# Performance work log

Hardware: AMD Instinct MI355X
Metric: run time of the kernel (lower is better)

## Reference

```python
import jax, jax.numpy as jnp
import numpy as np

B, CIN, COUT = 4, 64, 64
D, H, W = 8, 48, 48
KD = KH = KW = 3
K = KD * KH * KW  # 27 sampling taps
STRIDE, PAD, DIL = 1, 1, 1
KOFF, POFF = 3, 1
OFFSET_SCALE = 1.0


def setup_inputs() -> dict:
    key = jax.random.key(0)
    ks = jax.random.split(key, 7)
    x = jax.random.normal(ks[0], (B, CIN, D, H, W), jnp.float32)
    w_off = jax.random.normal(ks[1], (K * 3, CIN, KOFF, KOFF, KOFF), jnp.float32) * 0.01
    b_off = jax.random.normal(ks[2], (K * 3,), jnp.float32) * 0.01
    w_mask = jax.random.normal(ks[3], (K, CIN, KOFF, KOFF, KOFF), jnp.float32) * 0.05
    b_mask = jax.random.normal(ks[4], (K,), jnp.float32) * 0.05
    weight = jax.random.normal(ks[5], (COUT, CIN, KD, KH, KW), jnp.float32) * 0.02
    bias = jax.random.normal(ks[6], (COUT,), jnp.float32) * 0.02
    return dict(x=x, w_off=w_off, b_off=b_off, w_mask=w_mask, b_mask=b_mask,
                weight=weight, bias=bias)


def _conv3d(x, w, b, pad):
    out = jax.lax.conv_general_dilated(
        x, w, window_strides=(1, 1, 1), padding=[(pad, pad)] * 3,
        dimension_numbers=('NCDHW', 'OIDHW', 'NCDHW'))
    return out + b[None, :, None, None, None]


def _trilinear(x_flat, pz, py, px):
    # x_flat: [B, C, N]; pz/py/px: [B, N] fractional positions. Zero padding outside.
    z0, y0, x0 = jnp.floor(pz), jnp.floor(py), jnp.floor(px)
    acc = jnp.zeros_like(x_flat)
    for dz in (0.0, 1.0):
        for dy in (0.0, 1.0):
            for dx in (0.0, 1.0):
                zi, yi, xi = z0 + dz, y0 + dy, x0 + dx
                wgt = ((1.0 - jnp.abs(pz - zi)) * (1.0 - jnp.abs(py - yi))
                       * (1.0 - jnp.abs(px - xi)))
                valid = ((zi >= 0) & (zi < D) & (yi >= 0) & (yi < H)
                         & (xi >= 0) & (xi < W)).astype(x_flat.dtype)
                idx = ((jnp.clip(zi, 0, D - 1) * H + jnp.clip(yi, 0, H - 1)) * W
                       + jnp.clip(xi, 0, W - 1)).astype(jnp.int32)
                g = jnp.take_along_axis(x_flat, idx[:, None, :], axis=2)  # [B,C,N]
                acc = acc + g * (wgt * valid)[:, None, :]
    return acc


def reference(x, w_off, b_off, w_mask, b_mask, weight, bias):
    N = D * H * W
    # learned per-tap 3D offsets: [K, B, 3, N] ordered (dz, dy, dx)
    off = _conv3d(x, w_off, b_off, POFF).reshape(B, K, 3, N)
    off = jnp.transpose(off, (1, 0, 2, 3))
    # DCNv3-style attention mask: softmax over the K taps
    mask = jax.nn.softmax(_conv3d(x, w_mask, b_mask, POFF).reshape(B, K, N), axis=1)
    mask = jnp.transpose(mask, (1, 0, 2))  # [K, B, N]
    zo, yo, xo = jnp.meshgrid(jnp.arange(D, dtype=jnp.float32),
                              jnp.arange(H, dtype=jnp.float32),
                              jnp.arange(W, dtype=jnp.float32), indexing='ij')
    zo, yo, xo = zo.reshape(-1), yo.reshape(-1), xo.reshape(-1)  # [N]
    k_idx = jnp.arange(K)
    kz = (k_idx // (KH * KW)).astype(jnp.float32)
    ky = ((k_idx // KW) % KH).astype(jnp.float32)
    kx = (k_idx % KW).astype(jnp.float32)
    wk = jnp.transpose(weight.reshape(COUT, CIN, K), (2, 0, 1))  # [K, Cout, Cin]
    x_flat = x.reshape(B, CIN, N)

    def step(acc, inp):
        off_k, m_k, kzf, kyf, kxf, w_k = inp
        pz = zo[None] * STRIDE - PAD + kzf * DIL + OFFSET_SCALE * off_k[:, 0]
        py = yo[None] * STRIDE - PAD + kyf * DIL + OFFSET_SCALE * off_k[:, 1]
        px = xo[None] * STRIDE - PAD + kxf * DIL + OFFSET_SCALE * off_k[:, 2]
        s = _trilinear(x_flat, pz, py, px) * m_k[:, None, :]  # [B,Cin,N]
        return acc + jnp.einsum('oi,bin->bon', w_k, s), None

    acc0 = jnp.zeros((B, COUT, N), x.dtype)
    acc, _ = jax.lax.scan(step, acc0, (off, mask, kz, ky, kx, wk))
    return (acc + bias[None, :, None]).reshape(B, COUT, D, H, W)
```

## Files before the change

kernel.cpp:

```cpp
#include <hip/hip_runtime.h>
#include <hip/hip_bf16.h>
#include <math.h>

#define B_    4
#define CIN_  64
#define COUT_ 64
#define DD    8
#define HH    48
#define WW    48
#define HW2   (HH * WW)
#define NN    (DD * HH * WW)
#define BN    (B_ * NN)
#define KK    27
#define RS    116

typedef float f32x2 __attribute__((ext_vector_type(2)));
typedef float f32x4 __attribute__((ext_vector_type(4)));
typedef unsigned int u32x4 __attribute__((ext_vector_type(4)));
typedef __bf16 bf16x8 __attribute__((ext_vector_type(8)));
typedef __hip_bfloat16 bf16_t;

__device__ __forceinline__ float bflo(unsigned int u) {
  return __uint_as_float(u << 16);
}
__device__ __forceinline__ float bfhi(unsigned int u) {
  return __uint_as_float(u & 0xffff0000u);
}

__global__ __launch_bounds__(256) void init_kernel(
    const float* __restrict__ w_off, const float* __restrict__ w_mask,
    const float* __restrict__ weight, bf16_t* __restrict__ wB,
    bf16_t* __restrict__ wBd, bf16_t* __restrict__ zp)
{
  const int o = blockIdx.x * 256 + threadIdx.x;
  {
    const int ci = o & 63;
    const int ch = (o >> 6) % 112;
    const int k  = o / (112 * 64);
    float v = 0.f;
    if (ch < 81)       v = w_off[((size_t)ch * CIN_ + ci) * KK + k];
    else if (ch < 108) v = w_mask[((size_t)(ch - 81) * CIN_ + ci) * KK + k];
    wB[o] = __float2bfloat16(v);
  }
  if (o < KK * CIN_ * COUT_) {
    const int ci = o & 63;
    const int co = (o >> 6) & 63;
    const int k  = o >> 12;
    wBd[o] = __float2bfloat16(weight[((size_t)co * CIN_ + ci) * KK + k]);
  }
  if (o < 128) zp[o] = __float2bfloat16(0.f);
}

__global__ __launch_bounds__(256) void transpose_x_kernel(
    const float* __restrict__ x, bf16_t* __restrict__ xTbf)
{
  const int tid = threadIdx.x;
  const int n0  = blockIdx.x * 64;
  const int b   = blockIdx.y;
  __shared__ float tile[64][65];

  for (int i = tid; i < 4096; i += 256) {
    const int c  = i >> 6;
    const int nl = i & 63;
    tile[c][nl] = x[((size_t)(b * CIN_ + c)) * NN + n0 + nl];
  }
  __syncthreads();
  for (int i = tid; i < 4096; i += 256) {
    const int nl = i >> 6;
    const int c  = i & 63;
    xTbf[((size_t)(b * NN + n0 + nl)) * CIN_ + c] = __float2bfloat16(tile[c][nl]);
  }
}

__global__ __launch_bounds__(128) void fused_kernel(
    const bf16_t* __restrict__ xTbf, const bf16_t* __restrict__ wB,
    const float* __restrict__ b_off, const float* __restrict__ b_mask,
    const bf16_t* __restrict__ zp, const bf16_t* __restrict__ wBd,
    const float* __restrict__ bias, float* __restrict__ out)
{
  const int bid  = (blockIdx.x % 8) * 144 + blockIdx.x / 8;
  const int tid  = threadIdx.x;
  const int wid  = tid >> 6;
  const int lane = tid & 63;
  const int lg   = lane >> 4;
  const int lr   = lane & 15;

  const int tile = bid * 2 + wid;
  const int b    = tile / 576;
  const int rem  = tile % 576;
  const int z    = rem / 72;
  const int r2   = rem % 72;
  const int y0   = (r2 / 3) * 2;
  const int x0   = (r2 % 3) * 16;
  const int n0   = (z * HH + y0) * WW + x0;

  __shared__ float OM[2][32][RS];
  __shared__ __align__(16) unsigned short S[2][32][64];

  const bf16_t* xb = xTbf + (size_t)b * NN * CIN_;

  f32x4 acc[2][7];
#pragma unroll
  for (int mf = 0; mf < 2; ++mf)
#pragma unroll
    for (int nf = 0; nf < 7; ++nf) acc[mf][nf] = (f32x4){0.f, 0.f, 0.f, 0.f};

#pragma unroll 3
  for (int k = 0; k < KK; ++k) {
    const int kz = k / 9;
    const int kr = k - kz * 9;
    const int ky = kr / 3;
    const int kx = kr - ky * 3;

    bf16x8 afr[2][2];
    const int zz = z + kz - 1;
    const int xx = x0 + lr + kx - 1;
    const bool vzx = ((unsigned)zz < (unsigned)DD) & ((unsigned)xx < (unsigned)WW);
#pragma unroll
    for (int mf = 0; mf < 2; ++mf) {
      const int yy = y0 + mf + ky - 1;
      const bool v = vzx & ((unsigned)yy < (unsigned)HH);
      const bf16_t* ab = v ? (xb + (size_t)((zz * HH + yy) * WW + xx) * CIN_) : zp;
      afr[mf][0] = *(const bf16x8*)(ab + 8 * lg);
      afr[mf][1] = *(const bf16x8*)(ab + 32 + 8 * lg);
    }

    const bf16_t* wk = wB + (size_t)k * (112 * 64) + lr * 64 + 8 * lg;
#pragma unroll
    for (int nf = 0; nf < 7; ++nf) {
      const bf16x8 b0 = *(const bf16x8*)(wk + nf * 1024);
      const bf16x8 b1 = *(const bf16x8*)(wk + nf * 1024 + 32);
      acc[0][nf] = __builtin_amdgcn_mfma_f32_16x16x32_bf16(afr[0][0], b0, acc[0][nf], 0, 0, 0);
      acc[1][nf] = __builtin_amdgcn_mfma_f32_16x16x32_bf16(afr[1][0], b0, acc[1][nf], 0, 0, 0);
      acc[0][nf] = __builtin_amdgcn_mfma_f32_16x16x32_bf16(afr[0][1], b1, acc[0][nf], 0, 0, 0);
      acc[1][nf] = __builtin_amdgcn_mfma_f32_16x16x32_bf16(afr[1][1], b1, acc[1][nf], 0, 0, 0);
    }
  }

#pragma unroll
  for (int nf = 0; nf < 7; ++nf) {
    const int ch = 16 * nf + lr;
    if (ch < 108) {
      const float bv  = (ch < 81) ? b_off[ch] : b_mask[ch - 81];
      const int   slot = (ch < 81) ? (4 * (ch / 3) + (ch % 3)) : (4 * (ch - 81) + 3);
#pragma unroll
      for (int mf = 0; mf < 2; ++mf)
#pragma unroll
        for (int r = 0; r < 4; ++r)
          OM[wid][mf * 16 + 4 * lg + r][slot] = acc[mf][nf][r] + bv;
    }
  }
  __syncthreads();

  if (lane < 32) {
    const int pos = lane;
    float v[KK];
    float mx = -1e30f;
#pragma unroll
    for (int k = 0; k < KK; ++k) { v[k] = OM[wid][pos][4 * k + 3]; mx = fmaxf(mx, v[k]); }
    float s = 0.f;
#pragma unroll
    for (int k = 0; k < KK; ++k) { v[k] = expf(v[k] - mx); s += v[k]; }
    const float inv = 1.f / s;
#pragma unroll
    for (int k = 0; k < KK; ++k) OM[wid][pos][4 * k + 3] = v[k] * inv;
  }
  __syncthreads();

  const int p8 = lane >> 3;
  const int q  = lane & 7;

  const unsigned short* xq = (const unsigned short*)xb + (q << 3);
  unsigned short* Sw  = &S[wid][0][0];
  unsigned int*   SwU = (unsigned int*)Sw;

  float pxb[4], pyb[4];
#pragma unroll
  for (int oct = 0; oct < 4; ++oct) {
    const int j  = oct * 8 + p8;
    pyb[oct] = (float)(y0 + (j >> 4) - 1);
    pxb[oct] = (float)(x0 + (j & 15) - 1);
  }
  const float pzb = (float)(z - 1);

  f32x4 dacc[2][4];
#pragma unroll
  for (int mf = 0; mf < 2; ++mf)
#pragma unroll
    for (int nf = 0; nf < 4; ++nf) dacc[mf][nf] = (f32x4){0.f, 0.f, 0.f, 0.f};

#pragma unroll 2
  for (int k = 0; k < KK; ++k) {
    const int kz = k / 9;
    const int kr = k - kz * 9;
    const int ky = kr / 3;
    const int kx = kr - ky * 3;
    const float kzf = (float)kz, kyf = (float)ky, kxf = (float)kx;

#pragma unroll
    for (int oct = 0; oct < 4; ++oct) {
      const int j = oct * 8 + p8;
      const f32x4 om = *(const f32x4*)(&OM[wid][j][4 * k]);

      const float pz = pzb + kzf + om.x;
      const float py = pyb[oct] + kyf + om.y;
      const float px = pxb[oct] + kxf + om.z;
      const float m  = om.w;

      const float zf = floorf(pz); const float fz = pz - zf; const int z0 = (int)zf;
      const float yf = floorf(py); const float fy = py - yf; const int y0i = (int)yf;
      const float xf = floorf(px); const float fx = px - xf; const int xi0 = (int)xf;

      const float wz0 = ((unsigned)z0        < DD) ? (1.f - fz) : 0.f;
      const float wz1 = ((unsigned)(z0 + 1)  < DD) ? fz         : 0.f;
      const float wy0 = ((unsigned)y0i       < HH) ? (1.f - fy) : 0.f;
      const float wy1 = ((unsigned)(y0i + 1) < HH) ? fy         : 0.f;
      const float wx0 = ((unsigned)xi0       < WW) ? (1.f - fx) : 0.f;
      const float wx1 = ((unsigned)(xi0 + 1) < WW) ? fx         : 0.f;

      const int z0c = min(max(z0, 0),      DD - 1);
      const int z1c = min(max(z0 + 1, 0),  DD - 1);
      const int y0c = min(max(y0i, 0),     HH - 1);
      const int y1c = min(max(y0i + 1, 0), HH - 1);
      const int x0c = min(max(xi0, 0),     WW - 1);
      const int x1c = min(max(xi0 + 1, 0), WW - 1);

      const int r00 = (z0c * HH + y0c) * WW;
      const int r01 = (z0c * HH + y1c) * WW;
      const int r10 = (z1c * HH + y0c) * WW;
      const int r11 = (z1c * HH + y1c) * WW;

      const int rows[8] = {r00 + x0c, r00 + x1c, r01 + x0c, r01 + x1c,
                           r10 + x0c, r10 + x1c, r11 + x0c, r11 + x1c};
      const float w00 = wz0 * wy0, w01 = wz0 * wy1;
      const float w10 = wz1 * wy0, w11 = wz1 * wy1;
      const float wgt[8] = {w00 * wx0, w00 * wx1, w01 * wx0, w01 * wx1,
                            w10 * wx0, w10 * wx1, w11 * wx0, w11 * wx1};

      u32x4 cv[8];
#pragma unroll
      for (int c = 0; c < 8; ++c)
        cv[c] = *(const u32x4*)(xq + ((size_t)rows[c] << 6));

      f32x2 a01 = {0.f, 0.f}, a23 = {0.f, 0.f}, a45 = {0.f, 0.f}, a67 = {0.f, 0.f};
#pragma unroll
      for (int c = 0; c < 8; ++c) {
        const float w_ = wgt[c];
        a01 += (f32x2){bflo(cv[c].x), bfhi(cv[c].x)} * w_;
        a23 += (f32x2){bflo(cv[c].y), bfhi(cv[c].y)} * w_;
        a45 += (f32x2){bflo(cv[c].z), bfhi(cv[c].z)} * w_;
        a67 += (f32x2){bflo(cv[c].w), bfhi(cv[c].w)} * w_;
      }

      a01 *= m; a23 *= m; a45 *= m; a67 *= m;
      unsigned int d0, d1, d2, d3;
      asm("v_cvt_pk_bf16_f32 %0, %1, %2" : "=v"(d0) : "v"(a01.x), "v"(a01.y));
      asm("v_cvt_pk_bf16_f32 %0, %1, %2" : "=v"(d1) : "v"(a23.x), "v"(a23.y));
      asm("v_cvt_pk_bf16_f32 %0, %1, %2" : "=v"(d2) : "v"(a45.x), "v"(a45.y));
      asm("v_cvt_pk_bf16_f32 %0, %1, %2" : "=v"(d3) : "v"(a67.x), "v"(a67.y));
      const int slot = q ^ (j & 7);
      *(u32x4*)(SwU + j * 32 + slot * 4) = (u32x4){d0, d1, d2, d3};
    }

    bf16x8 afr2[2][2];
#pragma unroll
    for (int mf = 0; mf < 2; ++mf)
#pragma unroll
      for (int t2 = 0; t2 < 2; ++t2) {
        const int row  = 16 * mf + lr;
        const int slot = (t2 * 4 + lg) ^ (row & 7);
        afr2[mf][t2] = *(const bf16x8*)(Sw + row * 64 + slot * 8);
      }
    const bf16_t* wk = wBd + (size_t)k * 4096 + lr * 64 + 8 * lg;
#pragma unroll
    for (int nf = 0; nf < 4; ++nf) {
      const bf16x8 wv0 = *(const bf16x8*)(wk + nf * 1024);
      const bf16x8 wv1 = *(const bf16x8*)(wk + nf * 1024 + 32);
      dacc[0][nf] = __builtin_amdgcn_mfma_f32_16x16x32_bf16(afr2[0][0], wv0, dacc[0][nf], 0, 0, 0);
      dacc[1][nf] = __builtin_amdgcn_mfma_f32_16x16x32_bf16(afr2[1][0], wv0, dacc[1][nf], 0, 0, 0);
      dacc[0][nf] = __builtin_amdgcn_mfma_f32_16x16x32_bf16(afr2[0][1], wv1, dacc[0][nf], 0, 0, 0);
      dacc[1][nf] = __builtin_amdgcn_mfma_f32_16x16x32_bf16(afr2[1][1], wv1, dacc[1][nf], 0, 0, 0);
    }
  }

#pragma unroll
  for (int nf = 0; nf < 4; ++nf) {
    const float bv = bias[16 * nf + lr];
    float* op = out + ((size_t)(b * COUT_ + 16 * nf + lr)) * NN + n0 + 4 * lg;
#pragma unroll
    for (int mf = 0; mf < 2; ++mf)
      *(f32x4*)(op + mf * WW) = dacc[mf][nf] + bv;
  }
}

extern "C" void kernel_launch(void* const* d_in, const int* in_sizes, int n_in,
                              void* d_out, int out_size, void* d_ws, size_t ws_size,
                              hipStream_t stream)
{
  const float* x      = (const float*)d_in[0];
  const float* w_off  = (const float*)d_in[1];
  const float* b_off  = (const float*)d_in[2];
  const float* w_mask = (const float*)d_in[3];
  const float* b_mask = (const float*)d_in[4];
  const float* weight = (const float*)d_in[5];
  const float* bias   = (const float*)d_in[6];
  float* out = (float*)d_out;

  char* ws = (char*)d_ws;
  bf16_t* xTbf = (bf16_t*)ws;
  bf16_t* wB   = (bf16_t*)(ws + 9437184);
  bf16_t* wBd  = (bf16_t*)(ws + 9824256);
  bf16_t* zp   = (bf16_t*)(ws + 10045440);

  init_kernel<<<(KK * 112 * 64) / 256, 256, 0, stream>>>(w_off, w_mask, weight,
                                                         wB, wBd, zp);
  dim3 gtx(NN / 64, B_);
  transpose_x_kernel<<<gtx, 256, 0, stream>>>(x, xTbf);

  fused_kernel<<<1152, 128, 0, stream>>>(xTbf, wB, b_off, b_mask, zp, wBd,
                                         bias, out);
}
```

Measured before the change: 319.3 us.

## Halve per-wave tile to 16 positions and store offsets/mask as fp16 in LDS

Each wave now handles one 16-wide row segment instead of a 2x16 block, so the grid doubles to 2304 blocks and per-thread accumulators and fragments shrink by half. The offset/mask staging buffer moves from fp32 to fp16, which cuts shared-memory use. Together these lower register and LDS pressure to allow more resident waves and more parallelism. The cost is that each weight load from global memory now feeds half as many MFMAs, and the fp16 rounding of offsets and mask weights adds precision error.

```diff
diff --git a/kernel.cpp b/kernel.cpp
--- a/kernel.cpp
+++ b/kernel.cpp
@@ -12,10 +12,10 @@
 #define NN    (DD * HH * WW)
 #define BN    (B_ * NN)
 #define KK    27
-#define RS    116
 
 typedef float f32x2 __attribute__((ext_vector_type(2)));
 typedef float f32x4 __attribute__((ext_vector_type(4)));
+typedef unsigned int u32x2 __attribute__((ext_vector_type(2)));
 typedef unsigned int u32x4 __attribute__((ext_vector_type(4)));
 typedef __bf16 bf16x8 __attribute__((ext_vector_type(8)));
 typedef __hip_bfloat16 bf16_t;
@@ -25,6 +25,13 @@
 }
 __device__ __forceinline__ float bfhi(unsigned int u) {
   return __uint_as_float(u & 0xffff0000u);
+}
+__device__ __forceinline__ unsigned short f32_to_h(float x) {
+  _Float16 h = (_Float16)x;
+  return __builtin_bit_cast(unsigned short, h);
+}
+__device__ __forceinline__ float h_to_f32(unsigned short u) {
+  return (float)__builtin_bit_cast(_Float16, u);
 }
 
 __global__ __launch_bounds__(256) void init_kernel(
@@ -78,7 +85,7 @@
     const bf16_t* __restrict__ zp, const bf16_t* __restrict__ wBd,
     const float* __restrict__ bias, float* __restrict__ out)
 {
-  const int bid  = (blockIdx.x % 8) * 144 + blockIdx.x / 8;
+  const int bid  = (blockIdx.x % 8) * 288 + blockIdx.x / 8;
   const int tid  = threadIdx.x;
   const int wid  = tid >> 6;
   const int lane = tid & 63;
@@ -86,24 +93,22 @@
   const int lr   = lane & 15;
 
   const int tile = bid * 2 + wid;
-  const int b    = tile / 576;
-  const int rem  = tile % 576;
-  const int z    = rem / 72;
-  const int r2   = rem % 72;
-  const int y0   = (r2 / 3) * 2;
+  const int b    = tile / 1152;
+  const int rem  = tile % 1152;
+  const int z    = rem / 144;
+  const int r2   = rem % 144;
+  const int y    = r2 / 3;
   const int x0   = (r2 % 3) * 16;
-  const int n0   = (z * HH + y0) * WW + x0;
-
-  __shared__ float OM[2][32][RS];
-  __shared__ __align__(16) unsigned short S[2][32][64];
+  const int n0   = (z * HH + y) * WW + x0;
+
+  __shared__ __align__(16) unsigned short OMh[2][16][112];
+  __shared__ __align__(16) unsigned short S[2][16][64];
 
   const bf16_t* xb = xTbf + (size_t)b * NN * CIN_;
 
-  f32x4 acc[2][7];
-#pragma unroll
-  for (int mf = 0; mf < 2; ++mf)
-#pragma unroll
-    for (int nf = 0; nf < 7; ++nf) acc[mf][nf] = (f32x4){0.f, 0.f, 0.f, 0.f};
+  f32x4 acc[7];
+#pragma unroll
+  for (int nf = 0; nf < 7; ++nf) acc[nf] = (f32x4){0.f, 0.f, 0.f, 0.f};
 
 #pragma unroll 3
   for (int k = 0; k < KK; ++k) {
@@ -112,28 +117,23 @@
     const int ky = kr / 3;
     const int kx = kr - ky * 3;
 
-    bf16x8 afr[2][2];
     const int zz = z + kz - 1;
+    const int yy = y + ky - 1;
     const int xx = x0 + lr + kx - 1;
-    const bool vzx = ((unsigned)zz < (unsigned)DD) & ((unsigned)xx < (unsigned)WW);
-#pragma unroll
-    for (int mf = 0; mf < 2; ++mf) {
-      const int yy = y0 + mf + ky - 1;
-      const bool v = vzx & ((unsigned)yy < (unsigned)HH);
-      const bf16_t* ab = v ? (xb + (size_t)((zz * HH + yy) * WW + xx) * CIN_) : zp;
-      afr[mf][0] = *(const bf16x8*)(ab + 8 * lg);
-      afr[mf][1] = *(const bf16x8*)(ab + 32 + 8 * lg);
-    }
+    const bool v = ((unsigned)zz < (unsigned)DD) &
+                   ((unsigned)yy < (unsigned)HH) &
+                   ((unsigned)xx < (unsigned)WW);
+    const bf16_t* ab = v ? (xb + (size_t)((zz * HH + yy) * WW + xx) * CIN_) : zp;
+    const bf16x8 a0 = *(const bf16x8*)(ab + 8 * lg);
+    const bf16x8 a1 = *(const bf16x8*)(ab + 32 + 8 * lg);
 
     const bf16_t* wk = wB + (size_t)k * (112 * 64) + lr * 64 + 8 * lg;
 #pragma unroll
     for (int nf = 0; nf < 7; ++nf) {
       const bf16x8 b0 = *(const bf16x8*)(wk + nf * 1024);
       const bf16x8 b1 = *(const bf16x8*)(wk + nf * 1024 + 32);
-      acc[0][nf] = __builtin_amdgcn_mfma_f32_16x16x32_bf16(afr[0][0], b0, acc[0][nf], 0, 0, 0);
-      acc[1][nf] = __builtin_amdgcn_mfma_f32_16x16x32_bf16(afr[1][0], b0, acc[1][nf], 0, 0, 0);
-      acc[0][nf] = __builtin_amdgcn_mfma_f32_16x16x32_bf16(afr[0][1], b1, acc[0][nf], 0, 0, 0);
-      acc[1][nf] = __builtin_amdgcn_mfma_f32_16x16x32_bf16(afr[1][1], b1, acc[1][nf], 0, 0, 0);
+      acc[nf] = __builtin_amdgcn_mfma_f32_16x16x32_bf16(a0, b0, acc[nf], 0, 0, 0);
+      acc[nf] = __builtin_amdgcn_mfma_f32_16x16x32_bf16(a1, b1, acc[nf], 0, 0, 0);
     }
   }
 
@@ -141,29 +141,31 @@
   for (int nf = 0; nf < 7; ++nf) {
     const int ch = 16 * nf + lr;
     if (ch < 108) {
-      const float bv  = (ch < 81) ? b_off[ch] : b_mask[ch - 81];
+      const float bv   = (ch < 81) ? b_off[ch] : b_mask[ch - 81];
       const int   slot = (ch < 81) ? (4 * (ch / 3) + (ch % 3)) : (4 * (ch - 81) + 3);
 #pragma unroll
-      for (int mf = 0; mf < 2; ++mf)
-#pragma unroll
-        for (int r = 0; r < 4; ++r)
-          OM[wid][mf * 16 + 4 * lg + r][slot] = acc[mf][nf][r] + bv;
+      for (int r = 0; r < 4; ++r)
+        OMh[wid][4 * lg + r][slot] = f32_to_h(acc[nf][r] + bv);
     }
   }
   __syncthreads();
 
-  if (lane < 32) {
+  if (lane < 16) {
     const int pos = lane;
     float v[KK];
     float mx = -1e30f;
 #pragma unroll
-    for (int k = 0; k < KK; ++k) { v[k] = OM[wid][pos][4 * k + 3]; mx = fmaxf(mx, v[k]); }
+    for (int k = 0; k < KK; ++k) {
+      v[k] = h_to_f32(OMh[wid][pos][4 * k + 3]);
+      mx = fmaxf(mx, v[k]);
+    }
     float s = 0.f;
 #pragma unroll
     for (int k = 0; k < KK; ++k) { v[k] = expf(v[k] - mx); s += v[k]; }
     const float inv = 1.f / s;
 #pragma unroll
-    for (int k = 0; k < KK; ++k) OM[wid][pos][4 * k + 3] = v[k] * inv;
+    for (int k = 0; k < KK; ++k)
+      OMh[wid][pos][4 * k + 3] = f32_to_h(v[k] * inv);
   }
   __syncthreads();
 
@@ -174,20 +176,12 @@
   unsigned short* Sw  = &S[wid][0][0];
   unsigned int*   SwU = (unsigned int*)Sw;
 
-  float pxb[4], pyb[4];
-#pragma unroll
-  for (int oct = 0; oct < 4; ++oct) {
-    const int j  = oct * 8 + p8;
-    pyb[oct] = (float)(y0 + (j >> 4) - 1);
-    pxb[oct] = (float)(x0 + (j & 15) - 1);
-  }
   const float pzb = (float)(z - 1);
-
-  f32x4 dacc[2][4];
-#pragma unroll
-  for (int mf = 0; mf < 2; ++mf)
-#pragma unroll
-    for (int nf = 0; nf < 4; ++nf) dacc[mf][nf] = (f32x4){0.f, 0.f, 0.f, 0.f};
+  const float pyb = (float)(y - 1);
+
+  f32x4 dacc[4];
+#pragma unroll
+  for (int nf = 0; nf < 4; ++nf) dacc[nf] = (f32x4){0.f, 0.f, 0.f, 0.f};
 
 #pragma unroll 2
   for (int k = 0; k < KK; ++k) {
@@ -198,14 +192,17 @@
     const float kzf = (float)kz, kyf = (float)ky, kxf = (float)kx;
 
 #pragma unroll
-    for (int oct = 0; oct < 4; ++oct) {
+    for (int oct = 0; oct < 2; ++oct) {
       const int j = oct * 8 + p8;
-      const f32x4 om = *(const f32x4*)(&OM[wid][j][4 * k]);
-
-      const float pz = pzb + kzf + om.x;
-      const float py = pyb[oct] + kyf + om.y;
-      const float px = pxb[oct] + kxf + om.z;
-      const float m  = om.w;
+      const u32x2 omu = *(const u32x2*)(&OMh[wid][j][4 * k]);
+      const float oz = h_to_f32((unsigned short)(omu.x & 0xffff));
+      const float oy = h_to_f32((unsigned short)(omu.x >> 16));
+      const float ox = h_to_f32((unsigned short)(omu.y & 0xffff));
+      const float m  = h_to_f32((unsigned short)(omu.y >> 16));
+
+      const float pz = pzb + kzf + oz;
+      const float py = pyb + kyf + oy;
+      const float px = (float)(x0 + j - 1) + kxf + ox;
 
       const float zf = floorf(pz); const float fz = pz - zf; const int z0 = (int)zf;
       const float yf = floorf(py); const float fy = py - yf; const int y0i = (int)yf;
@@ -258,28 +255,23 @@
       asm("v_cvt_pk_bf16_f32 %0, %1, %2" : "=v"(d1) : "v"(a23.x), "v"(a23.y));
       asm("v_cvt_pk_bf16_f32 %0, %1, %2" : "=v"(d2) : "v"(a45.x), "v"(a45.y));
       asm("v_cvt_pk_bf16_f32 %0, %1, %2" : "=v"(d3) : "v"(a67.x), "v"(a67.y));
-      const int slot = q ^ (j & 7);
+      const int slot = q ^ p8;
       *(u32x4*)(SwU + j * 32 + slot * 4) = (u32x4){d0, d1, d2, d3};
     }
 
-    bf16x8 afr2[2][2];
-#pragma unroll
-    for (int mf = 0; mf < 2; ++mf)
-#pragma unroll
-      for (int t2 = 0; t2 < 2; ++t2) {
-        const int row  = 16 * mf + lr;
-        const int slot = (t2 * 4 + lg) ^ (row & 7);
-        afr2[mf][t2] = *(const bf16x8*)(Sw + row * 64 + slot * 8);
-      }
+    bf16x8 afr[2];
+#pragma unroll
+    for (int t2 = 0; t2 < 2; ++t2) {
+      const int slot = (t2 * 4 + lg) ^ (lr & 7);
+      afr[t2] = *(const bf16x8*)(Sw + lr * 64 + slot * 8);
+    }
     const bf16_t* wk = wBd + (size_t)k * 4096 + lr * 64 + 8 * lg;
 #pragma unroll
     for (int nf = 0; nf < 4; ++nf) {
       const bf16x8 wv0 = *(const bf16x8*)(wk + nf * 1024);
       const bf16x8 wv1 = *(const bf16x8*)(wk + nf * 1024 + 32);
-      dacc[0][nf] = __builtin_amdgcn_mfma_f32_16x16x32_bf16(afr2[0][0], wv0, dacc[0][nf], 0, 0, 0);
-      dacc[1][nf] = __builtin_amdgcn_mfma_f32_16x16x32_bf16(afr2[1][0], wv0, dacc[1][nf], 0, 0, 0);
-      dacc[0][nf] = __builtin_amdgcn_mfma_f32_16x16x32_bf16(afr2[0][1], wv1, dacc[0][nf], 0, 0, 0);
-      dacc[1][nf] = __builtin_amdgcn_mfma_f32_16x16x32_bf16(afr2[1][1], wv1, dacc[1][nf], 0, 0, 0);
+      dacc[nf] = __builtin_amdgcn_mfma_f32_16x16x32_bf16(afr[0], wv0, dacc[nf], 0, 0, 0);
+      dacc[nf] = __builtin_amdgcn_mfma_f32_16x16x32_bf16(afr[1], wv1, dacc[nf], 0, 0, 0);
     }
   }
 
@@ -287,9 +279,7 @@
   for (int nf = 0; nf < 4; ++nf) {
     const float bv = bias[16 * nf + lr];
     float* op = out + ((size_t)(b * COUT_ + 16 * nf + lr)) * NN + n0 + 4 * lg;
-#pragma unroll
-    for (int mf = 0; mf < 2; ++mf)
-      *(f32x4*)(op + mf * WW) = dacc[mf][nf] + bv;
+    *(f32x4*)op = dacc[nf] + bv;
   }
 }
 
@@ -317,6 +307,6 @@
   dim3 gtx(NN / 64, B_);
   transpose_x_kernel<<<gtx, 256, 0, stream>>>(x, xTbf);
 
-  fused_kernel<<<1152, 128, 0, stream>>>(xTbf, wB, b_off, b_mask, zp, wBd,
+  fused_kernel<<<2304, 128, 0, stream>>>(xTbf, wB, b_off, b_mask, zp, wBd,
                                          bias, out);
 }
```

Measured after the change: 431.5 us. 1.35x slower.

## Split each tile's 27 taps across two waves with shared-memory reduction

Applied to the files above, without the earlier changes.

Each block now handles a single 32-position tile rather than two. Its two waves split the 27 kernel taps between them, 14 and 13, for both the offset/mask convolution and the deformable sampling GEMM. Partial sums are combined through LDS: wave 1 adds into the offset buffer wave 0 wrote, and for the output wave 1 stores its partial accumulators that wave 0 adds before writing. This doubles the grid to 2304 blocks for more parallelism and shorter per-wave serial chains. The cost is extra barriers and LDS reduction traffic, and each block now does half the work.

```diff
diff --git a/kernel.cpp b/kernel.cpp
--- a/kernel.cpp
+++ b/kernel.cpp
@@ -78,27 +78,32 @@
     const bf16_t* __restrict__ zp, const bf16_t* __restrict__ wBd,
     const float* __restrict__ bias, float* __restrict__ out)
 {
-  const int bid  = (blockIdx.x % 8) * 144 + blockIdx.x / 8;
+  const int bid  = (blockIdx.x % 8) * 288 + blockIdx.x / 8;
   const int tid  = threadIdx.x;
   const int wid  = tid >> 6;
   const int lane = tid & 63;
   const int lg   = lane >> 4;
   const int lr   = lane & 15;
 
-  const int tile = bid * 2 + wid;
-  const int b    = tile / 576;
-  const int rem  = tile % 576;
+  const int b    = bid / 576;
+  const int rem  = bid % 576;
   const int z    = rem / 72;
   const int r2   = rem % 72;
   const int y0   = (r2 / 3) * 2;
   const int x0   = (r2 % 3) * 16;
   const int n0   = (z * HH + y0) * WW + x0;
 
-  __shared__ float OM[2][32][RS];
-  __shared__ __align__(16) unsigned short S[2][32][64];
+  __shared__ float OM[32][RS];
+  __shared__ __align__(16) char SPu[9216];
+  unsigned short* Sw  = (unsigned short*)SPu + wid * 2048;
+  unsigned int*   SwU = (unsigned int*)Sw;
+  float*          Pp  = (float*)SPu;
 
   const bf16_t* xb = xTbf + (size_t)b * NN * CIN_;
 
+  const int ck0 = wid ? 14 : 0;
+  const int ck1 = wid ? 27 : 14;
+
   f32x4 acc[2][7];
 #pragma unroll
   for (int mf = 0; mf < 2; ++mf)
@@ -106,7 +111,7 @@
     for (int nf = 0; nf < 7; ++nf) acc[mf][nf] = (f32x4){0.f, 0.f, 0.f, 0.f};
 
 #pragma unroll 3
-  for (int k = 0; k < KK; ++k) {
+  for (int k = ck0; k < ck1; ++k) {
     const int kz = k / 9;
     const int kr = k - kz * 9;
     const int ky = kr / 3;
@@ -137,33 +142,50 @@
     }
   }
 
-#pragma unroll
-  for (int nf = 0; nf < 7; ++nf) {
-    const int ch = 16 * nf + lr;
-    if (ch < 108) {
-      const float bv  = (ch < 81) ? b_off[ch] : b_mask[ch - 81];
-      const int   slot = (ch < 81) ? (4 * (ch / 3) + (ch % 3)) : (4 * (ch - 81) + 3);
-#pragma unroll
-      for (int mf = 0; mf < 2; ++mf)
-#pragma unroll
-        for (int r = 0; r < 4; ++r)
-          OM[wid][mf * 16 + 4 * lg + r][slot] = acc[mf][nf][r] + bv;
-    }
-  }
-  __syncthreads();
-
-  if (lane < 32) {
-    const int pos = lane;
+  if (wid == 0) {
+#pragma unroll
+    for (int nf = 0; nf < 7; ++nf) {
+      const int ch = 16 * nf + lr;
+      if (ch < 108) {
+        const float bv   = (ch < 81) ? b_off[ch] : b_mask[ch - 81];
+        const int   slot = (ch < 81) ? (4 * (ch / 3) + (ch % 3)) : (4 * (ch - 81) + 3);
+#pragma unroll
+        for (int mf = 0; mf < 2; ++mf)
+#pragma unroll
+          for (int r = 0; r < 4; ++r)
+            OM[mf * 16 + 4 * lg + r][slot] = acc[mf][nf][r] + bv;
+      }
+    }
+  }
+  __syncthreads();
+  if (wid == 1) {
+#pragma unroll
+    for (int nf = 0; nf < 7; ++nf) {
+      const int ch = 16 * nf + lr;
+      if (ch < 108) {
+        const int slot = (ch < 81) ? (4 * (ch / 3) + (ch % 3)) : (4 * (ch - 81) + 3);
+#pragma unroll
+        for (int mf = 0; mf < 2; ++mf)
+#pragma unroll
+          for (int r = 0; r < 4; ++r)
+            OM[mf * 16 + 4 * lg + r][slot] += acc[mf][nf][r];
+      }
+    }
+  }
+  __syncthreads();
+
+  if (lane < 16) {
+    const int pos = wid * 16 + lane;
     float v[KK];
     float mx = -1e30f;
 #pragma unroll
-    for (int k = 0; k < KK; ++k) { v[k] = OM[wid][pos][4 * k + 3]; mx = fmaxf(mx, v[k]); }
+    for (int k = 0; k < KK; ++k) { v[k] = OM[pos][4 * k + 3]; mx = fmaxf(mx, v[k]); }
     float s = 0.f;
 #pragma unroll
     for (int k = 0; k < KK; ++k) { v[k] = expf(v[k] - mx); s += v[k]; }
     const float inv = 1.f / s;
 #pragma unroll
-    for (int k = 0; k < KK; ++k) OM[wid][pos][4 * k + 3] = v[k] * inv;
+    for (int k = 0; k < KK; ++k) OM[pos][4 * k + 3] = v[k] * inv;
   }
   __syncthreads();
 
@@ -171,8 +193,6 @@
   const int q  = lane & 7;
 
   const unsigned short* xq = (const unsigned short*)xb + (q << 3);
-  unsigned short* Sw  = &S[wid][0][0];
-  unsigned int*   SwU = (unsigned int*)Sw;
 
   float pxb[4], pyb[4];
 #pragma unroll
@@ -183,6 +203,9 @@
   }
   const float pzb = (float)(z - 1);
 
+  const int dk0 = wid ? 14 : 0;
+  const int dkN = wid ? 13 : 14;
+
   f32x4 dacc[2][4];
 #pragma unroll
   for (int mf = 0; mf < 2; ++mf)
@@ -190,7 +213,8 @@
     for (int nf = 0; nf < 4; ++nf) dacc[mf][nf] = (f32x4){0.f, 0.f, 0.f, 0.f};
 
 #pragma unroll 2
-  for (int k = 0; k < KK; ++k) {
+  for (int t = 0; t < dkN; ++t) {
+    const int k  = dk0 + t;
     const int kz = k / 9;
     const int kr = k - kz * 9;
     const int ky = kr / 3;
@@ -200,7 +224,7 @@
 #pragma unroll
     for (int oct = 0; oct < 4; ++oct) {
       const int j = oct * 8 + p8;
-      const f32x4 om = *(const f32x4*)(&OM[wid][j][4 * k]);
+      const f32x4 om = *(const f32x4*)(&OM[j][4 * k]);
 
       const float pz = pzb + kzf + om.x;
       const float py = pyb[oct] + kyf + om.y;
@@ -283,13 +307,26 @@
     }
   }
 
-#pragma unroll
-  for (int nf = 0; nf < 4; ++nf) {
-    const float bv = bias[16 * nf + lr];
-    float* op = out + ((size_t)(b * COUT_ + 16 * nf + lr)) * NN + n0 + 4 * lg;
-#pragma unroll
-    for (int mf = 0; mf < 2; ++mf)
-      *(f32x4*)(op + mf * WW) = dacc[mf][nf] + bv;
+  __syncthreads();
+  if (wid == 1) {
+#pragma unroll
+    for (int nf = 0; nf < 4; ++nf)
+#pragma unroll
+      for (int mf = 0; mf < 2; ++mf)
+        *(f32x4*)(Pp + (16 * nf + lr) * 36 + 16 * mf + 4 * lg) = dacc[mf][nf];
+  }
+  __syncthreads();
+  if (wid == 0) {
+#pragma unroll
+    for (int nf = 0; nf < 4; ++nf) {
+      const float bv = bias[16 * nf + lr];
+      float* op = out + ((size_t)(b * COUT_ + 16 * nf + lr)) * NN + n0 + 4 * lg;
+#pragma unroll
+      for (int mf = 0; mf < 2; ++mf) {
+        const f32x4 p = *(const f32x4*)(Pp + (16 * nf + lr) * 36 + 16 * mf + 4 * lg);
+        *(f32x4*)(op + mf * WW) = dacc[mf][nf] + p + bv;
+      }
+    }
   }
 }
 
@@ -317,6 +354,6 @@
   dim3 gtx(NN / 64, B_);
   transpose_x_kernel<<<gtx, 256, 0, stream>>>(x, xTbf);
 
-  fused_kernel<<<1152, 128, 0, stream>>>(xTbf, wB, b_off, b_mask, zp, wBd,
+  fused_kernel<<<2304, 128, 0, stream>>>(xTbf, wB, b_off, b_mask, zp, wBd,
                                          bias, out);
 }
```

After: 279.7 us (median of 2 runs). 12.4% less time.
